# Performance work log

Measured on AMD Instinct MI355X. Metric: run time of the kernel, lower is better.

The kernel has to match this reference:

```python
import jax, jax.numpy as jnp
import numpy as np

N_NODES = 100000
N_EDGES = 1600000
N_GRAPHS = 512
IN_C, HID, OUT_C = 128, 128, 64


def gcn_conv(x, W, b, src, dst, num_nodes):
    # PyG GCNConv: add self-loops, symmetric normalization D^-1/2 (A+I) D^-1/2, then linear.
    h = x @ W  # [N, F_out]
    deg = jnp.ones((num_nodes,), h.dtype).at[dst].add(jnp.ones((src.shape[0],), h.dtype))  # +1 for self-loop
    dinv = jax.lax.rsqrt(deg)
    norm = dinv[src] * dinv[dst]  # [E]
    agg = jnp.zeros_like(h).at[dst].add(h[src] * norm[:, None])
    agg = agg + h * (dinv * dinv)[:, None]  # self-loop contribution
    return agg + b


def global_mean_pool(x, batch, num_graphs):
    s = jax.ops.segment_sum(x, batch, num_segments=num_graphs)
    cnt = jax.ops.segment_sum(jnp.ones((x.shape[0],), x.dtype), batch, num_segments=num_graphs)
    return s / jnp.maximum(cnt, 1.0)[:, None]


def setup_inputs() -> dict:
    key = jax.random.key(0)
    ks = jax.random.split(key, 16)
    glorot = lambda k, i, o: jax.random.normal(k, (i, o), jnp.float32) * (2.0 / (i + o)) ** 0.5
    inp = {
        "x": jax.random.normal(ks[0], (N_NODES, IN_C), jnp.float32),
        "edge_index": jax.random.randint(ks[1], (2, N_EDGES), 0, N_NODES, jnp.int64 if jax.config.jax_enable_x64 else jnp.int32),
        "batch": jnp.sort(jax.random.randint(ks[2], (N_NODES,), 0, N_GRAPHS)),
        "W1": glorot(ks[3], IN_C, HID), "b1": jnp.zeros((HID,), jnp.float32),
        "W2": glorot(ks[4], HID, HID), "b2": jnp.zeros((HID,), jnp.float32),
        "W3": glorot(ks[5], HID, HID), "b3": jnp.zeros((HID,), jnp.float32),
        "Wf1": glorot(ks[6], HID, HID * 4), "bf1": jnp.zeros((HID * 4,), jnp.float32),
        "Wf2": glorot(ks[7], HID * 4, HID * 2), "bf2": jnp.zeros((HID * 2,), jnp.float32),
        "Wf3": glorot(ks[8], HID * 2, HID), "bf3": jnp.zeros((HID,), jnp.float32),
        "Wf4": glorot(ks[9], HID, OUT_C), "bf4": jnp.zeros((OUT_C,), jnp.float32),
    }
    return inp


def reference(x, edge_index, batch, W1, b1, W2, b2, W3, b3,
              Wf1, bf1, Wf2, bf2, Wf3, bf3, Wf4, bf4):
    src, dst = edge_index[0], edge_index[1]
    h = jax.nn.relu(gcn_conv(x, W1, b1, src, dst, N_NODES))
    h = jax.nn.relu(gcn_conv(h, W2, b2, src, dst, N_NODES))
    h = gcn_conv(h, W3, b3, src, dst, N_NODES)
    f = global_mean_pool(h, batch, N_GRAPHS)  # [G, HID]
    z = jax.nn.relu(f @ Wf1 + bf1)
    z = jax.nn.relu(z @ Wf2 + bf2)
    z = jax.nn.relu(z @ Wf3 + bf3)
    z = z @ Wf4 + bf4
    return (f, z)
```

## Files before the change

### kernel.cpp

```cpp
#include <hip/hip_runtime.h>
#include <hip/hip_bf16.h>

#define NN 100000
#define NE 1600000
#define NG 512
#define HID 128
#define NBLK 98
#define PPART 391
#define EPB 4096

typedef __attribute__((ext_vector_type(8))) short short8;
typedef __attribute__((ext_vector_type(4))) float floatx4;

__device__ inline ushort f2bf(float f) {
  uint u = __float_as_uint(f);
  u += 0x7fff + ((u >> 16) & 1);
  return (ushort)(u >> 16);
}
__device__ inline uint pack2(float lo, float hi) {
  return (uint)f2bf(lo) | ((uint)f2bf(hi) << 16);
}
__device__ inline float bflo(uint u) { return __uint_as_float(u << 16); }
__device__ inline float bfhi(uint u) { return __uint_as_float(u & 0xffff0000u); }

__global__ void k_count(const int* __restrict__ dst, int* __restrict__ cnt) {
  int e = blockIdx.x * 256 + threadIdx.x;
  if (e < NE) atomicAdd(&cnt[dst[e]], 1);
}

__global__ __launch_bounds__(1024) void k_scan1(const int* __restrict__ cnt,
                                                int* __restrict__ offs,
                                                int* __restrict__ bsum) {
  __shared__ int wsum[16];
  int t = threadIdx.x, lane = t & 63, wid = t >> 6;
  int i = blockIdx.x * 1024 + t;
  int v = (i < NN) ? cnt[i] : 0;
  int iv = v;
  for (int o = 1; o < 64; o <<= 1) {
    int n = __shfl_up(iv, o, 64);
    if (lane >= o) iv += n;
  }
  if (lane == 63) wsum[wid] = iv;
  __syncthreads();
  if (wid == 0 && lane < 16) {
    int w = wsum[lane];
    for (int o = 1; o < 16; o <<= 1) {
      int n = __shfl_up(w, o, 64);
      if (lane >= o) w += n;
    }
    wsum[lane] = w;
  }
  __syncthreads();
  int excl = iv - v + (wid ? wsum[wid - 1] : 0);
  if (i < NN) offs[i] = excl;
  if (t == 0) bsum[blockIdx.x] = wsum[15];
}

__global__ void k_scan2(int* __restrict__ bsum) {
  if (threadIdx.x == 0) {
    int run = 0;
    for (int b = 0; b < NBLK; ++b) {
      int v = bsum[b];
      bsum[b] = run;
      run += v;
    }
    bsum[NBLK] = run;
  }
}

__global__ __launch_bounds__(1024) void k_scan3(const int* __restrict__ cnt,
                                                int* __restrict__ offs,
                                                const int* __restrict__ bsum,
                                                float* __restrict__ dinv) {
  int i = blockIdx.x * 1024 + threadIdx.x;
  if (i < NN) {
    int o = offs[i] + bsum[blockIdx.x];
    offs[i] = o;
    dinv[i] = 1.0f / sqrtf((float)(cnt[i] + 1));
  }
  if (i == NN - 1) offs[NN] = bsum[NBLK];
}

__global__ void k_pinit(const int* __restrict__ offsets, int* __restrict__ pcur) {
  int p = blockIdx.x * 256 + threadIdx.x;
  if (p < PPART) pcur[p] = offsets[p << 8];
}

__global__ __launch_bounds__(256) void k_part(const int* __restrict__ src,
                                              const int* __restrict__ dst,
                                              int* __restrict__ pcur,
                                              uint* __restrict__ pedge) {
  __shared__ int hist[PPART];
  __shared__ int base[PPART];
  int t = threadIdx.x;
  for (int i = t; i < PPART; i += 256) hist[i] = 0;
  __syncthreads();
  int e0 = blockIdx.x * EPB;
  int d_[16];
#pragma unroll
  for (int l = 0; l < 16; ++l) {
    int e = e0 + l * 256 + t;
    if (e < NE) {
      int d = dst[e];
      d_[l] = d;
      atomicAdd(&hist[d >> 8], 1);
    } else {
      d_[l] = -1;
    }
  }
  __syncthreads();
  for (int i = t; i < PPART; i += 256) {
    int h = hist[i];
    base[i] = h ? atomicAdd(&pcur[i], h) : 0;
  }
  __syncthreads();
#pragma unroll
  for (int l = 0; l < 16; ++l) {
    int e = e0 + l * 256 + t;
    if (e < NE) {
      int d = d_[l];
      int s = src[e];
      int pos = atomicAdd(&base[d >> 8], 1);
      pedge[pos] = (uint)s | ((uint)(d & 255) << 24);
    }
  }
}

__global__ __launch_bounds__(256) void k_bucket2(const int* __restrict__ offsets,
                                                 const uint* __restrict__ pedge,
                                                 int* __restrict__ srcs) {
  __shared__ int cur[256];
  int p = blockIdx.x;
  int n0 = p << 8;
  int t = threadIdx.x;
  int hi = n0 + 256; if (hi > NN) hi = NN;
  if (n0 + t < hi) cur[t] = offsets[n0 + t];
  __syncthreads();
  int s = offsets[n0];
  int e = offsets[hi];
  for (int i = s + t; i < e; i += 256) {
    uint v = pedge[i];
    int pos = atomicAdd(&cur[v >> 24], 1);
    srcs[pos] = (int)(v & 0xFFFFFFu);
  }
}

__global__ void k_cast(const float4* __restrict__ x, uint2* __restrict__ xb, int n4) {
  int i = blockIdx.x * 256 + threadIdx.x;
  if (i < n4) {
    float4 v = x[i];
    uint2 o;
    o.x = pack2(v.x, v.y);
    o.y = pack2(v.z, v.w);
    xb[i] = o;
  }
}

__global__ __launch_bounds__(128) void k_prepW(const float* __restrict__ W,
                                               ushort* __restrict__ wt) {
  int c = blockIdx.x;
  int r = threadIdx.x;
  float v = W[r * 128 + c];
  wt[c * 128 + (((r >> 3) ^ (c & 15)) << 3) + (r & 7)] = f2bf(v);
}

__global__ __launch_bounds__(256) void k_gemm(const ushort* __restrict__ Xb,
                                              const ushort* __restrict__ wt,
                                              ushort* __restrict__ Hb) {
  __shared__ ushort sW[128 * 128];
  int t = threadIdx.x;
#pragma unroll
  for (int l = 0; l < 8; ++l) {
    int idx = t + l * 256;
    ((uint4*)sW)[idx] = ((const uint4*)wt)[idx];
  }
  __syncthreads();
  int wid = t >> 6, lane = t & 63;
  int row0 = blockIdx.x * 64 + wid * 16;
  int arow = row0 + (lane & 15);
  if (arow >= NN) arow = NN - 1;
  const ushort* aptr = Xb + (size_t)arow * 128 + ((lane >> 4) * 8);
  floatx4 acc[8];
#pragma unroll
  for (int n = 0; n < 8; ++n) acc[n] = (floatx4)(0.f);
#pragma unroll
  for (int kb = 0; kb < 4; ++kb) {
    short8 a = *(const short8*)(aptr + kb * 32);
    int kslot = kb * 4 + (lane >> 4);
#pragma unroll
    for (int n = 0; n < 8; ++n) {
      int col = n * 16 + (lane & 15);
      const ushort* bp = sW + col * 128 + ((kslot ^ (col & 15)) << 3);
      short8 b = *(const short8*)bp;
      acc[n] = __builtin_amdgcn_mfma_f32_16x16x32_bf16(a, b, acc[n], 0, 0, 0);
    }
  }
  int srow_base = row0 + (lane >> 4) * 4;
#pragma unroll
  for (int r = 0; r < 4; ++r) {
    int grow = srow_base + r;
    if (grow < NN) {
      ushort* out = Hb + (size_t)grow * 128 + (lane & 15);
#pragma unroll
      for (int n = 0; n < 8; ++n) out[n * 16] = f2bf(acc[n][r]);
    }
  }
}

__global__ __launch_bounds__(256) void k_agg(const ushort* __restrict__ H,
                                             const float* __restrict__ bias,
                                             const float* __restrict__ dinv,
                                             const int* __restrict__ offsets,
                                             const int* __restrict__ srcs,
                                             ushort* __restrict__ Hout, int do_relu) {
  int node = blockIdx.x * 16 + (threadIdx.x >> 4);
  if (node >= NN) return;
  int c8 = threadIdx.x & 15;
  float di = dinv[node];
  int s = offsets[node], e = offsets[node + 1];
  float acc[8];
#pragma unroll
  for (int j = 0; j < 8; ++j) acc[j] = 0.f;
  int i = s;
  for (; i + 7 < e; i += 8) {
    int sx[8];
    float dx[8];
    uint4 vx[8];
#pragma unroll
    for (int u = 0; u < 8; ++u) sx[u] = srcs[i + u];
#pragma unroll
    for (int u = 0; u < 8; ++u) dx[u] = dinv[sx[u]];
#pragma unroll
    for (int u = 0; u < 8; ++u) vx[u] = *((const uint4*)(H + (size_t)sx[u] * 128) + c8);
#pragma unroll
    for (int u = 0; u < 8; ++u) {
      acc[0] += bflo(vx[u].x) * dx[u];
      acc[1] += bfhi(vx[u].x) * dx[u];
      acc[2] += bflo(vx[u].y) * dx[u];
      acc[3] += bfhi(vx[u].y) * dx[u];
      acc[4] += bflo(vx[u].z) * dx[u];
      acc[5] += bfhi(vx[u].z) * dx[u];
      acc[6] += bflo(vx[u].w) * dx[u];
      acc[7] += bfhi(vx[u].w) * dx[u];
    }
  }
  for (; i < e; ++i) {
    int s0 = srcs[i];
    float d0 = dinv[s0];
    uint4 v0 = *((const uint4*)(H + (size_t)s0 * 128) + c8);
    acc[0] += bflo(v0.x) * d0;
    acc[1] += bfhi(v0.x) * d0;
    acc[2] += bflo(v0.y) * d0;
    acc[3] += bfhi(v0.y) * d0;
    acc[4] += bflo(v0.z) * d0;
    acc[5] += bfhi(v0.z) * d0;
    acc[6] += bflo(v0.w) * d0;
    acc[7] += bfhi(v0.w) * d0;
  }
  uint4 hv = *((const uint4*)(H + (size_t)node * 128) + c8);
  float hb[8] = {bflo(hv.x), bfhi(hv.x), bflo(hv.y), bfhi(hv.y),
                 bflo(hv.z), bfhi(hv.z), bflo(hv.w), bfhi(hv.w)};
  float dii = di * di;
  const float* bp = bias + c8 * 8;
  float r[8];
#pragma unroll
  for (int j = 0; j < 8; ++j) {
    float v = acc[j] * di + hb[j] * dii + bp[j];
    if (do_relu) v = fmaxf(v, 0.f);
    r[j] = v;
  }
  uint4 o;
  o.x = pack2(r[0], r[1]);
  o.y = pack2(r[2], r[3]);
  o.z = pack2(r[4], r[5]);
  o.w = pack2(r[6], r[7]);
  *((uint4*)(Hout + (size_t)node * 128) + c8) = o;
}

__device__ inline int lower_bound(const int* a, int n, int v) {
  int lo = 0, hi = n;
  while (lo < hi) {
    int m = (lo + hi) >> 1;
    if (a[m] < v) lo = m + 1; else hi = m;
  }
  return lo;
}

__global__ __launch_bounds__(128) void k_pool(const ushort* __restrict__ H,
                                              const int* __restrict__ batch,
                                              float* __restrict__ f) {
  int g = blockIdx.x;
  int c = threadIdx.x;
  int s = lower_bound(batch, NN, g);
  int e = lower_bound(batch, NN, g + 1);
  float acc = 0.f;
#pragma unroll 4
  for (int i = s; i < e; ++i)
    acc += __uint_as_float(((uint)H[(size_t)i * 128 + c]) << 16);
  f[g * 128 + c] = acc / fmaxf((float)(e - s), 1.0f);
}

__global__ __launch_bounds__(256) void k_mgemm(const float* __restrict__ X,
                                               const float* __restrict__ W,
                                               const float* __restrict__ bias,
                                               float* __restrict__ Y,
                                               int M, int K, int N, int do_relu) {
  __shared__ float sA[32][64];
  __shared__ float sB[32][64];
  int t = threadIdx.x;
  int tn = t & 15, tm = t >> 4;
  int m0 = blockIdx.y * 64;
  int n0 = blockIdx.x * 64;
  float acc[4][4];
#pragma unroll
  for (int i = 0; i < 4; ++i)
#pragma unroll
    for (int j = 0; j < 4; ++j) acc[i][j] = 0.f;

  for (int kb = 0; kb < K; kb += 32) {
#pragma unroll
    for (int l = 0; l < 2; ++l) {
      int idx = t * 2 + l;
      int r = idx >> 3, kq = idx & 7;
      float4 v = *(const float4*)(X + (size_t)(m0 + r) * K + kb + kq * 4);
      sA[kq * 4 + 0][r] = v.x;
      sA[kq * 4 + 1][r] = v.y;
      sA[kq * 4 + 2][r] = v.z;
      sA[kq * 4 + 3][r] = v.w;
    }
#pragma unroll
    for (int l = 0; l < 2; ++l) {
      int idx = t * 2 + l;
      int kr = idx >> 4, nq = idx & 15;
      *(float4*)&sB[kr][nq * 4] = *(const float4*)(W + (size_t)(kb + kr) * N + n0 + nq * 4);
    }
    __syncthreads();
#pragma unroll
    for (int k = 0; k < 32; ++k) {
      float a[4], b[4];
      *(float4*)a = *(float4*)&sA[k][tm * 4];
      *(float4*)b = *(float4*)&sB[k][tn * 4];
#pragma unroll
      for (int i = 0; i < 4; ++i)
#pragma unroll
        for (int j = 0; j < 4; ++j) acc[i][j] += a[i] * b[j];
    }
    __syncthreads();
  }
  float4 bv = *(const float4*)(bias + n0 + tn * 4);
#pragma unroll
  for (int i = 0; i < 4; ++i) {
    float4 o;
    o.x = acc[i][0] + bv.x;
    o.y = acc[i][1] + bv.y;
    o.z = acc[i][2] + bv.z;
    o.w = acc[i][3] + bv.w;
    if (do_relu) {
      o.x = fmaxf(o.x, 0.f);
      o.y = fmaxf(o.y, 0.f);
      o.z = fmaxf(o.z, 0.f);
      o.w = fmaxf(o.w, 0.f);
    }
    *(float4*)(Y + (size_t)(m0 + tm * 4 + i) * N + n0 + tn * 4) = o;
  }
}

extern "C" void kernel_launch(void* const* d_in, const int* in_sizes, int n_in,
                              void* d_out, int out_size, void* d_ws, size_t ws_size,
                              hipStream_t stream) {
  const float* x    = (const float*)d_in[0];
  const int* ei     = (const int*)d_in[1];
  const int* batch  = (const int*)d_in[2];
  const float* W1   = (const float*)d_in[3];  const float* b1  = (const float*)d_in[4];
  const float* W2   = (const float*)d_in[5];  const float* b2  = (const float*)d_in[6];
  const float* W3   = (const float*)d_in[7];  const float* b3  = (const float*)d_in[8];
  const float* Wf1  = (const float*)d_in[9];  const float* bf1 = (const float*)d_in[10];
  const float* Wf2  = (const float*)d_in[11]; const float* bf2 = (const float*)d_in[12];
  const float* Wf3  = (const float*)d_in[13]; const float* bf3 = (const float*)d_in[14];
  const float* Wf4  = (const float*)d_in[15]; const float* bf4 = (const float*)d_in[16];
  const int* src = ei;
  const int* dst = ei + NE;

  char* ws = (char*)d_ws;
  size_t off = 0;
  auto alloc = [&](size_t bytes) {
    void* p = ws + off;
    off += (bytes + 255) & ~(size_t)255;
    return p;
  };
  ushort* B0     = (ushort*)alloc((size_t)NN * 128 * 2);
  ushort* B1     = (ushort*)alloc((size_t)NN * 128 * 2);
  ushort* B2     = (ushort*)alloc((size_t)NN * 128 * 2);
  float* dinv    = (float*)alloc((size_t)NN * 4);
  int*   cnt     = (int*)alloc((size_t)NN * 4);
  int*   offsets = (int*)alloc((size_t)(NN + 1) * 4);
  int*   srcs    = (int*)alloc((size_t)NE * 4);
  uint*  pedge   = (uint*)alloc((size_t)NE * 4);
  int*   pcur    = (int*)alloc((size_t)PPART * 4);
  int*   bsum    = (int*)alloc((size_t)(NBLK + 1) * 4);
  ushort* wt1    = (ushort*)alloc(128 * 128 * 2);
  ushort* wt2    = (ushort*)alloc(128 * 128 * 2);
  ushort* wt3    = (ushort*)alloc(128 * 128 * 2);
  float* t1      = (float*)alloc((size_t)NG * 512 * 4);
  float* t2      = (float*)alloc((size_t)NG * 256 * 4);
  float* t3      = (float*)alloc((size_t)NG * 128 * 4);

  float* f_out = (float*)d_out;
  float* z_out = (float*)d_out + NG * HID;

  hipMemsetAsync(cnt, 0, (size_t)NN * 4, stream);
  k_count<<<(NE + 255) / 256, 256, 0, stream>>>(dst, cnt);
  k_scan1<<<NBLK, 1024, 0, stream>>>(cnt, offsets, bsum);
  k_scan2<<<1, 64, 0, stream>>>(bsum);
  k_scan3<<<NBLK, 1024, 0, stream>>>(cnt, offsets, bsum, dinv);
  k_pinit<<<(PPART + 255) / 256, 256, 0, stream>>>(offsets, pcur);
  k_part<<<(NE + EPB - 1) / EPB, 256, 0, stream>>>(src, dst, pcur, pedge);
  k_bucket2<<<PPART, 256, 0, stream>>>(offsets, pedge, srcs);

  k_prepW<<<128, 128, 0, stream>>>(W1, wt1);
  k_prepW<<<128, 128, 0, stream>>>(W2, wt2);
  k_prepW<<<128, 128, 0, stream>>>(W3, wt3);
  k_cast<<<(NN * 128 / 4 + 255) / 256, 256, 0, stream>>>((const float4*)x, (uint2*)B0, NN * 128 / 4);

  int gemm_grid = (NN + 63) / 64;
  int agg_grid = (NN + 15) / 16;

  k_gemm<<<gemm_grid, 256, 0, stream>>>(B0, wt1, B1);
  k_agg<<<agg_grid, 256, 0, stream>>>(B1, b1, dinv, offsets, srcs, B2, 1);
  k_gemm<<<gemm_grid, 256, 0, stream>>>(B2, wt2, B1);
  k_agg<<<agg_grid, 256, 0, stream>>>(B1, b2, dinv, offsets, srcs, B0, 1);
  k_gemm<<<gemm_grid, 256, 0, stream>>>(B0, wt3, B1);
  k_agg<<<agg_grid, 256, 0, stream>>>(B1, b3, dinv, offsets, srcs, B2, 0);

  k_pool<<<NG, 128, 0, stream>>>(B2, batch, f_out);

  k_mgemm<<<dim3(8, 8), 256, 0, stream>>>(f_out, Wf1, bf1, t1, NG, 128, 512, 1);
  k_mgemm<<<dim3(4, 8), 256, 0, stream>>>(t1, Wf2, bf2, t2, NG, 512, 256, 1);
  k_mgemm<<<dim3(2, 8), 256, 0, stream>>>(t2, Wf3, bf3, t3, NG, 256, 128, 1);
  k_mgemm<<<dim3(1, 8), 256, 0, stream>>>(t3, Wf4, bf4, z_out, NG, 128, 64, 0);
}
```

Measured before the change: 458.3 us.

## Build CSR via partition histogram and per-bucket local scan, halve MLP GEMM tiles

Replaces the per-node global atomic degree count and three-kernel node-level scan with a shared-memory partition histogram, a single-block partition scan, and a per-bucket local count/scan inside the bucketing kernel that also writes offsets and dinv. This removes 1.6M global atomics on a 100K-entry array and several launches. It also shrinks the MLP GEMM row tile from 64 to 32 to double the block count for the small head GEMMs. The cost is an extra pass over pedge inside each bucket block.

```diff
diff --git a/kernel.cpp b/kernel.cpp
--- a/kernel.cpp
+++ b/kernel.cpp
@@ -5,7 +5,6 @@
 #define NE 1600000
 #define NG 512
 #define HID 128
-#define NBLK 98
 #define PPART 391
 #define EPB 4096
 
@@ -23,67 +22,50 @@
 __device__ inline float bflo(uint u) { return __uint_as_float(u << 16); }
 __device__ inline float bfhi(uint u) { return __uint_as_float(u & 0xffff0000u); }
 
-__global__ void k_count(const int* __restrict__ dst, int* __restrict__ cnt) {
-  int e = blockIdx.x * 256 + threadIdx.x;
-  if (e < NE) atomicAdd(&cnt[dst[e]], 1);
-}
-
-__global__ __launch_bounds__(1024) void k_scan1(const int* __restrict__ cnt,
-                                                int* __restrict__ offs,
-                                                int* __restrict__ bsum) {
-  __shared__ int wsum[16];
+__global__ __launch_bounds__(256) void k_hist(const int* __restrict__ dst,
+                                              int* __restrict__ phist) {
+  __shared__ int h[PPART];
+  int t = threadIdx.x;
+  for (int i = t; i < PPART; i += 256) h[i] = 0;
+  __syncthreads();
+  int e0 = blockIdx.x * EPB;
+#pragma unroll
+  for (int l = 0; l < 16; ++l) {
+    int e = e0 + l * 256 + t;
+    if (e < NE) atomicAdd(&h[dst[e] >> 8], 1);
+  }
+  __syncthreads();
+  for (int i = t; i < PPART; i += 256)
+    if (h[i]) atomicAdd(&phist[i], h[i]);
+}
+
+__global__ __launch_bounds__(512) void k_pscan(const int* __restrict__ phist,
+                                               int* __restrict__ pbase) {
+  __shared__ int ws[8];
   int t = threadIdx.x, lane = t & 63, wid = t >> 6;
-  int i = blockIdx.x * 1024 + t;
-  int v = (i < NN) ? cnt[i] : 0;
+  int v = (t < PPART) ? phist[t] : 0;
   int iv = v;
   for (int o = 1; o < 64; o <<= 1) {
     int n = __shfl_up(iv, o, 64);
     if (lane >= o) iv += n;
   }
-  if (lane == 63) wsum[wid] = iv;
-  __syncthreads();
-  if (wid == 0 && lane < 16) {
-    int w = wsum[lane];
-    for (int o = 1; o < 16; o <<= 1) {
-      int n = __shfl_up(w, o, 64);
-      if (lane >= o) w += n;
-    }
-    wsum[lane] = w;
-  }
-  __syncthreads();
-  int excl = iv - v + (wid ? wsum[wid - 1] : 0);
-  if (i < NN) offs[i] = excl;
-  if (t == 0) bsum[blockIdx.x] = wsum[15];
-}
-
-__global__ void k_scan2(int* __restrict__ bsum) {
-  if (threadIdx.x == 0) {
-    int run = 0;
-    for (int b = 0; b < NBLK; ++b) {
-      int v = bsum[b];
-      bsum[b] = run;
-      run += v;
-    }
-    bsum[NBLK] = run;
-  }
-}
-
-__global__ __launch_bounds__(1024) void k_scan3(const int* __restrict__ cnt,
-                                                int* __restrict__ offs,
-                                                const int* __restrict__ bsum,
-                                                float* __restrict__ dinv) {
-  int i = blockIdx.x * 1024 + threadIdx.x;
-  if (i < NN) {
-    int o = offs[i] + bsum[blockIdx.x];
-    offs[i] = o;
-    dinv[i] = 1.0f / sqrtf((float)(cnt[i] + 1));
-  }
-  if (i == NN - 1) offs[NN] = bsum[NBLK];
-}
-
-__global__ void k_pinit(const int* __restrict__ offsets, int* __restrict__ pcur) {
+  if (lane == 63) ws[wid] = iv;
+  __syncthreads();
+  int add = 0;
+#pragma unroll
+  for (int w = 0; w < 8; ++w) add += (w < wid) ? ws[w] : 0;
+  if (t < PPART) pbase[t] = iv - v + add;
+  if (t == 0) {
+    int tot = 0;
+#pragma unroll
+    for (int w = 0; w < 8; ++w) tot += ws[w];
+    pbase[PPART] = tot;
+  }
+}
+
+__global__ void k_pinit(const int* __restrict__ pbase, int* __restrict__ pcur) {
   int p = blockIdx.x * 256 + threadIdx.x;
-  if (p < PPART) pcur[p] = offsets[p << 8];
+  if (p < PPART) pcur[p] = pbase[p];
 }
 
 __global__ __launch_bounds__(256) void k_part(const int* __restrict__ src,
@@ -126,22 +108,48 @@
   }
 }
 
-__global__ __launch_bounds__(256) void k_bucket2(const int* __restrict__ offsets,
+__global__ __launch_bounds__(256) void k_bucket2(const int* __restrict__ pbase,
                                                  const uint* __restrict__ pedge,
-                                                 int* __restrict__ srcs) {
+                                                 int* __restrict__ srcs,
+                                                 int* __restrict__ offsets,
+                                                 float* __restrict__ dinv) {
+  __shared__ int cnt_s[256];
   __shared__ int cur[256];
+  __shared__ int ws[4];
   int p = blockIdx.x;
   int n0 = p << 8;
   int t = threadIdx.x;
-  int hi = n0 + 256; if (hi > NN) hi = NN;
-  if (n0 + t < hi) cur[t] = offsets[n0 + t];
-  __syncthreads();
-  int s = offsets[n0];
-  int e = offsets[hi];
+  int lim = NN - n0; if (lim > 256) lim = 256;
+  int s = pbase[p], e = pbase[p + 1];
+  cnt_s[t] = 0;
+  __syncthreads();
+  for (int i = s + t; i < e; i += 256) atomicAdd(&cnt_s[pedge[i] >> 24], 1);
+  __syncthreads();
+  int v = cnt_s[t];
+  int lane = t & 63, wid = t >> 6;
+  int iv = v;
+  for (int o = 1; o < 64; o <<= 1) {
+    int n = __shfl_up(iv, o, 64);
+    if (lane >= o) iv += n;
+  }
+  if (lane == 63) ws[wid] = iv;
+  __syncthreads();
+  int add = 0;
+#pragma unroll
+  for (int w = 0; w < 4; ++w) add += (w < wid) ? ws[w] : 0;
+  int excl = iv - v + add;
+  if (t < lim) {
+    int o = s + excl;
+    offsets[n0 + t] = o;
+    cur[t] = o;
+    dinv[n0 + t] = 1.0f / sqrtf((float)(v + 1));
+  }
+  if (p == PPART - 1 && t == 0) offsets[NN] = NE;
+  __syncthreads();
   for (int i = s + t; i < e; i += 256) {
-    uint v = pedge[i];
-    int pos = atomicAdd(&cur[v >> 24], 1);
-    srcs[pos] = (int)(v & 0xFFFFFFu);
+    uint pv = pedge[i];
+    int pos = atomicAdd(&cur[pv >> 24], 1);
+    srcs[pos] = (int)(pv & 0xFFFFFFu);
   }
 }
 
@@ -265,9 +273,9 @@
   float r[8];
 #pragma unroll
   for (int j = 0; j < 8; ++j) {
-    float v = acc[j] * di + hb[j] * dii + bp[j];
-    if (do_relu) v = fmaxf(v, 0.f);
-    r[j] = v;
+    float vv = acc[j] * di + hb[j] * dii + bp[j];
+    if (do_relu) vv = fmaxf(vv, 0.f);
+    r[j] = vv;
   }
   uint4 o;
   o.x = pack2(r[0], r[1]);
@@ -305,23 +313,21 @@
                                                const float* __restrict__ bias,
                                                float* __restrict__ Y,
                                                int M, int K, int N, int do_relu) {
-  __shared__ float sA[32][64];
+  __shared__ float sA[32][32];
   __shared__ float sB[32][64];
   int t = threadIdx.x;
   int tn = t & 15, tm = t >> 4;
-  int m0 = blockIdx.y * 64;
+  int m0 = blockIdx.y * 32;
   int n0 = blockIdx.x * 64;
-  float acc[4][4];
-#pragma unroll
-  for (int i = 0; i < 4; ++i)
+  float acc[2][4];
+#pragma unroll
+  for (int i = 0; i < 2; ++i)
 #pragma unroll
     for (int j = 0; j < 4; ++j) acc[i][j] = 0.f;
 
   for (int kb = 0; kb < K; kb += 32) {
-#pragma unroll
-    for (int l = 0; l < 2; ++l) {
-      int idx = t * 2 + l;
-      int r = idx >> 3, kq = idx & 7;
+    {
+      int r = t >> 3, kq = t & 7;
       float4 v = *(const float4*)(X + (size_t)(m0 + r) * K + kb + kq * 4);
       sA[kq * 4 + 0][r] = v.x;
       sA[kq * 4 + 1][r] = v.y;
@@ -337,11 +343,12 @@
     __syncthreads();
 #pragma unroll
     for (int k = 0; k < 32; ++k) {
-      float a[4], b[4];
-      *(float4*)a = *(float4*)&sA[k][tm * 4];
+      float a[2], b[4];
+      a[0] = sA[k][tm * 2];
+      a[1] = sA[k][tm * 2 + 1];
       *(float4*)b = *(float4*)&sB[k][tn * 4];
 #pragma unroll
-      for (int i = 0; i < 4; ++i)
+      for (int i = 0; i < 2; ++i)
 #pragma unroll
         for (int j = 0; j < 4; ++j) acc[i][j] += a[i] * b[j];
     }
@@ -349,7 +356,7 @@
   }
   float4 bv = *(const float4*)(bias + n0 + tn * 4);
 #pragma unroll
-  for (int i = 0; i < 4; ++i) {
+  for (int i = 0; i < 2; ++i) {
     float4 o;
     o.x = acc[i][0] + bv.x;
     o.y = acc[i][1] + bv.y;
@@ -361,7 +368,7 @@
       o.z = fmaxf(o.z, 0.f);
       o.w = fmaxf(o.w, 0.f);
     }
-    *(float4*)(Y + (size_t)(m0 + tm * 4 + i) * N + n0 + tn * 4) = o;
+    *(float4*)(Y + (size_t)(m0 + tm * 2 + i) * N + n0 + tn * 4) = o;
   }
 }
 
@@ -392,12 +399,12 @@
   ushort* B1     = (ushort*)alloc((size_t)NN * 128 * 2);
   ushort* B2     = (ushort*)alloc((size_t)NN * 128 * 2);
   float* dinv    = (float*)alloc((size_t)NN * 4);
-  int*   cnt     = (int*)alloc((size_t)NN * 4);
   int*   offsets = (int*)alloc((size_t)(NN + 1) * 4);
   int*   srcs    = (int*)alloc((size_t)NE * 4);
   uint*  pedge   = (uint*)alloc((size_t)NE * 4);
+  int*   phist   = (int*)alloc((size_t)PPART * 4);
+  int*   pbase   = (int*)alloc((size_t)(PPART + 1) * 4);
   int*   pcur    = (int*)alloc((size_t)PPART * 4);
-  int*   bsum    = (int*)alloc((size_t)(NBLK + 1) * 4);
   ushort* wt1    = (ushort*)alloc(128 * 128 * 2);
   ushort* wt2    = (ushort*)alloc(128 * 128 * 2);
   ushort* wt3    = (ushort*)alloc(128 * 128 * 2);
@@ -408,14 +415,12 @@
   float* f_out = (float*)d_out;
   float* z_out = (float*)d_out + NG * HID;
 
-  hipMemsetAsync(cnt, 0, (size_t)NN * 4, stream);
-  k_count<<<(NE + 255) / 256, 256, 0, stream>>>(dst, cnt);
-  k_scan1<<<NBLK, 1024, 0, stream>>>(cnt, offsets, bsum);
-  k_scan2<<<1, 64, 0, stream>>>(bsum);
-  k_scan3<<<NBLK, 1024, 0, stream>>>(cnt, offsets, bsum, dinv);
-  k_pinit<<<(PPART + 255) / 256, 256, 0, stream>>>(offsets, pcur);
+  hipMemsetAsync(phist, 0, (size_t)PPART * 4, stream);
+  k_hist<<<(NE + EPB - 1) / EPB, 256, 0, stream>>>(dst, phist);
+  k_pscan<<<1, 512, 0, stream>>>(phist, pbase);
+  k_pinit<<<(PPART + 255) / 256, 256, 0, stream>>>(pbase, pcur);
   k_part<<<(NE + EPB - 1) / EPB, 256, 0, stream>>>(src, dst, pcur, pedge);
-  k_bucket2<<<PPART, 256, 0, stream>>>(offsets, pedge, srcs);
+  k_bucket2<<<PPART, 256, 0, stream>>>(pbase, pedge, srcs, offsets, dinv);
 
   k_prepW<<<128, 128, 0, stream>>>(W1, wt1);
   k_prepW<<<128, 128, 0, stream>>>(W2, wt2);
@@ -434,8 +439,8 @@
 
   k_pool<<<NG, 128, 0, stream>>>(B2, batch, f_out);
 
-  k_mgemm<<<dim3(8, 8), 256, 0, stream>>>(f_out, Wf1, bf1, t1, NG, 128, 512, 1);
-  k_mgemm<<<dim3(4, 8), 256, 0, stream>>>(t1, Wf2, bf2, t2, NG, 512, 256, 1);
-  k_mgemm<<<dim3(2, 8), 256, 0, stream>>>(t2, Wf3, bf3, t3, NG, 256, 128, 1);
-  k_mgemm<<<dim3(1, 8), 256, 0, stream>>>(t3, Wf4, bf4, z_out, NG, 128, 64, 0);
-}
+  k_mgemm<<<dim3(8, 16), 256, 0, stream>>>(f_out, Wf1, bf1, t1, NG, 128, 512, 1);
+  k_mgemm<<<dim3(4, 16), 256, 0, stream>>>(t1, Wf2, bf2, t2, NG, 512, 256, 1);
+  k_mgemm<<<dim3(2, 16), 256, 0, stream>>>(t2, Wf3, bf3, t3, NG, 256, 128, 1);
+  k_mgemm<<<dim3(1, 16), 256, 0, stream>>>(t3, Wf4, bf4, z_out, NG, 128, 64, 0);
+}
```

Measured after the change: 387.5 us. 1.18x faster.
